# Kernel tuning notes

Measured on AMD Instinct MI355X. Metric: run time of the kernel, lower is better.

The kernel has to match this reference:

```python
import jax, jax.numpy as jnp
import numpy as np

D_MODEL, N_HEADS, D_HEAD = 768, 12, 64
BATCH, SEQ = 4, 2048
INIT_STD = 0.02


def setup_inputs() -> dict:
    key = jax.random.key(0)
    ks = jax.random.split(key, 5)
    x = jax.random.normal(ks[0], (BATCH, SEQ, D_MODEL), dtype=jnp.float32)
    W_Q = INIT_STD * jax.random.normal(ks[1], (N_HEADS, D_MODEL, D_HEAD), dtype=jnp.float32)
    W_K = INIT_STD * jax.random.normal(ks[2], (N_HEADS, D_MODEL, D_HEAD), dtype=jnp.float32)
    W_V = INIT_STD * jax.random.normal(ks[3], (N_HEADS, D_MODEL, D_HEAD), dtype=jnp.float32)
    W_O = INIT_STD * jax.random.normal(ks[4], (N_HEADS, D_HEAD, D_MODEL), dtype=jnp.float32)
    b_Q = jnp.zeros((N_HEADS, D_HEAD), dtype=jnp.float32)
    b_K = jnp.zeros((N_HEADS, D_HEAD), dtype=jnp.float32)
    b_V = jnp.zeros((N_HEADS, D_HEAD), dtype=jnp.float32)
    b_O = jnp.zeros((D_MODEL,), dtype=jnp.float32)
    return {"x": x, "W_Q": W_Q, "W_K": W_K, "W_V": W_V, "W_O": W_O,
            "b_Q": b_Q, "b_K": b_K, "b_V": b_V, "b_O": b_O}


def reference(x, W_Q, W_K, W_V, W_O, b_Q, b_K, b_V, b_O):
    # projections: [b,s,e] x [n,e,h] -> [b,s,n,h]
    q = jnp.einsum('bse,neh->bsnh', x, W_Q) + b_Q
    k = jnp.einsum('bse,neh->bsnh', x, W_K) + b_K
    v = jnp.einsum('bse,neh->bsnh', x, W_V) + b_V
    scores = jnp.einsum('bqnh,bknh->bnqk', q, k) / np.float32(np.sqrt(D_HEAD))
    S = x.shape[1]
    causal = jnp.tril(jnp.ones((S, S), dtype=bool))  # True where allowed
    scores = jnp.where(causal, scores, -jnp.inf)
    pattern = jax.nn.softmax(scores, axis=-1)
    z = jnp.einsum('bnqk,bknh->bqnh', pattern, v)
    # combine heads: sum over n of z @ W_O
    attn_out = jnp.einsum('bqnh,nhe->bqe', z, W_O) + b_O
    return attn_out
```

## Files before the change

kernel.cpp:

```cpp
#include <hip/hip_runtime.h>
#include <hip/hip_bf16.h>

typedef short s16x8 __attribute__((ext_vector_type(8)));
typedef short s16x4 __attribute__((ext_vector_type(4)));
typedef float f32x4 __attribute__((ext_vector_type(4)));
typedef __hip_bfloat16 bf16;

#define MFMA16(a, b, c) __builtin_amdgcn_mfma_f32_16x16x32_bf16((a), (b), (c), 0, 0, 0)

#define BATCH 4
#define SEQ 2048
#define NH 12
#define DH 64
#define DM 768
#define ROWS (BATCH * SEQ)
#define QKVC (3 * DM)
#define LOG2E 1.4426950408889634f

static __device__ inline float fast_exp2(float x) {
  float r;
  asm("v_exp_f32 %0, %1" : "=v"(r) : "v"(x));
  return r;
}
static __device__ inline unsigned pkbf16(float a, float b) {
  bf16 ha = __float2bfloat16(a), hb = __float2bfloat16(b);
  unsigned short ua, ub;
  __builtin_memcpy(&ua, &ha, 2);
  __builtin_memcpy(&ub, &hb, 2);
  return (unsigned)ua | ((unsigned)ub << 16);
}

typedef __attribute__((address_space(3))) unsigned int lds_u32;
typedef __attribute__((address_space(1))) const unsigned int glb_u32;
static __device__ inline void gl2lds16(const void* g, void* l) {
  __builtin_amdgcn_global_load_lds((glb_u32*)g, (lds_u32*)l, 16, 0, 0);
}

#define NWC (QKVC * DM)
#define NWO (DM * DM)
#define NXC (ROWS * DM / 8)
__global__ __launch_bounds__(256) void prep_all(
    const float* __restrict__ wq, const float* __restrict__ wk,
    const float* __restrict__ wv, const float* __restrict__ wo,
    const float* __restrict__ x, bf16* __restrict__ WcT,
    bf16* __restrict__ WoT, bf16* __restrict__ xb) {
  int i = blockIdx.x * 256 + threadIdx.x;
  if (i < NWC) {
    int c = i / DM, e = i % DM;
    int mat = c / DM;
    int r = c % DM;
    int n = r >> 6, h = r & 63;
    const float* W = (mat == 0) ? wq : ((mat == 1) ? wk : wv);
    WcT[i] = __float2bfloat16(W[n * (DM * DH) + e * DH + h]);
  } else if (i < NWC + NWO) {
    int j = i - NWC;
    int e = j / DM, r = j % DM;
    WoT[j] = __float2bfloat16(wo[r * DM + e]);
  } else {
    int j = i - NWC - NWO;
    const float* src = x + (size_t)j * 8;
    float4 f0 = *(const float4*)src;
    float4 f1 = *(const float4*)(src + 4);
    bf16 tmp[8];
    tmp[0] = __float2bfloat16(f0.x); tmp[1] = __float2bfloat16(f0.y);
    tmp[2] = __float2bfloat16(f0.z); tmp[3] = __float2bfloat16(f0.w);
    tmp[4] = __float2bfloat16(f1.x); tmp[5] = __float2bfloat16(f1.y);
    tmp[6] = __float2bfloat16(f1.z); tmp[7] = __float2bfloat16(f1.w);
    *(s16x8*)(xb + (size_t)j * 8) = *(const s16x8*)tmp;
  }
}

__global__ __launch_bounds__(256) void qkv_gemm(
    const bf16* __restrict__ xb, const bf16* __restrict__ WcT,
    const float* __restrict__ bQ, const float* __restrict__ bK,
    const float* __restrict__ bV, bf16* __restrict__ Qb,
    bf16* __restrict__ Kb, bf16* __restrict__ Vt) {
  __shared__ bf16 As[128 * 32];
  __shared__ bf16 Bs[128 * 32];
  const int m0 = blockIdx.x * 128;
  const int n0 = blockIdx.y * 128;
  const int tid = threadIdx.x;
  const int wave = tid >> 6, lane = tid & 63;
  const int quad = lane >> 4, l15 = lane & 15;
  const int wm = (wave & 1) * 64, wn = (wave >> 1) * 64;

  f32x4 acc[4][4] = {};

  for (int k0 = 0; k0 < DM; k0 += 32) {
    {
      int c = tid, row = c >> 2, sg = (c & 3) << 3;
      gl2lds16(xb + (size_t)(m0 + row) * DM + k0 + sg, &As[c * 8]);
      gl2lds16(WcT + (size_t)(n0 + row) * DM + k0 + sg, &Bs[c * 8]);
      c = tid + 256; row = c >> 2; sg = (c & 3) << 3;
      gl2lds16(xb + (size_t)(m0 + row) * DM + k0 + sg, &As[c * 8]);
      gl2lds16(WcT + (size_t)(n0 + row) * DM + k0 + sg, &Bs[c * 8]);
    }
    __syncthreads();
    s16x8 af[4], bfr[4];
    for (int i = 0; i < 4; i++)
      af[i] = *(const s16x8*)&As[(wm + i * 16 + l15) * 32 + quad * 8];
    for (int j = 0; j < 4; j++)
      bfr[j] = *(const s16x8*)&Bs[(wn + j * 16 + l15) * 32 + quad * 8];
    for (int i = 0; i < 4; i++)
      for (int j = 0; j < 4; j++)
        acc[i][j] = MFMA16(af[i], bfr[j], acc[i][j]);
    __syncthreads();
  }

  const int mat = n0 / DM;
  for (int j = 0; j < 4; j++) {
    int col = n0 + wn + j * 16 + l15;
    int cc = col - mat * DM;
    int head = cc >> 6, h = cc & 63;
    float bsv = ((mat == 0) ? bQ : (mat == 1) ? bK : bV)[cc];
    for (int i = 0; i < 4; i++) {
      int row0 = m0 + wm + i * 16 + quad * 4;
      int b = row0 >> 11;
      int s = row0 & 2047;
      int bh = b * NH + head;
      if (mat == 2) {
        s16x4 pv;
        for (int r = 0; r < 4; r++) {
          bf16 hv = __float2bfloat16(acc[i][j][r] + bsv);
          short sv; __builtin_memcpy(&sv, &hv, 2);
          pv[r] = sv;
        }
        *(s16x4*)(Vt + ((size_t)bh * DH + h) * SEQ + s) = pv;
      } else {
        const float scale = (mat == 0) ? (0.125f * LOG2E) : 1.0f;
        bf16* dst = ((mat == 0) ? Qb : Kb) + ((size_t)bh * SEQ + s) * DH + h;
        for (int r = 0; r < 4; r++)
          dst[(size_t)r * DH] = __float2bfloat16((acc[i][j][r] + bsv) * scale);
      }
    }
  }
}

__global__ __launch_bounds__(256) void flash_kernel(
    const bf16* __restrict__ Qb, const bf16* __restrict__ Kb,
    const bf16* __restrict__ Vt, bf16* __restrict__ Z) {
  __shared__ bf16 Ks[64 * 72];
  __shared__ bf16 VsT[64 * 72];
  __shared__ bf16 Ps[4][16 * 72];

  const int bh = blockIdx.x >> 4;
  const int p = blockIdx.x & 15;
  const int qtA = 31 - p, qtB = p;
  const int b = bh / NH, head = bh % NH;
  const int tid = threadIdx.x;
  const int wave = tid >> 6, lane = tid & 63;
  const int quad = lane >> 4, l15 = lane & 15;
  const int qwA = qtA * 64 + wave * 16;
  const int qwB = qtB * 64 + wave * 16;

  const bf16* Kbase = Kb + (size_t)bh * SEQ * DH;
  const bf16* Vbase = Vt + (size_t)bh * DH * SEQ;

  s16x8 bqA[2], bqB[2];
  for (int ks = 0; ks < 2; ks++) {
    bqA[ks] = *(const s16x8*)(Qb +
        ((size_t)bh * SEQ + qwA + l15) * DH + ks * 32 + quad * 8);
    bqB[ks] = *(const s16x8*)(Qb +
        ((size_t)bh * SEQ + qwB + l15) * DH + ks * 32 + quad * 8);
  }

  f32x4 oA[4] = {}, oB[4] = {};
  float lA = 0.f, lB = 0.f;

  s16x8 kr[2], vr[2];
  auto load_tile = [&](int kt) {
    const int kbase = kt * 64;
    for (int u = 0; u < 2; u++) {
      int c = tid + u * 256;
      int row = c >> 3, seg = (c & 7) << 3;
      kr[u] = *(const s16x8*)(Kbase + (size_t)(kbase + row) * DH + seg);
      vr[u] = *(const s16x8*)(Vbase + (size_t)row * SEQ + kbase + seg);
    }
  };
  auto store_tile = [&]() {
    for (int u = 0; u < 2; u++) {
      int c = tid + u * 256;
      int row = c >> 3, seg = (c & 7) << 3;
      *(s16x8*)&Ks[row * 72 + seg] = kr[u];
      *(s16x8*)&VsT[row * 72 + seg] = vr[u];
    }
  };

  auto compute = [&](int kt, const s16x8 bq[2], f32x4 o[4], float& l_i,
                     int qw, bool diag) {
    const int kbase = kt * 64;
    f32x4 s[4] = {};
    for (int ks = 0; ks < 2; ks++) {
      s16x8 ak[4];
      for (int ktf = 0; ktf < 4; ktf++)
        ak[ktf] = *(const s16x8*)&Ks[(ktf * 16 + l15) * 72 + ks * 32 + quad * 8];
      for (int ktf = 0; ktf < 4; ktf++)
        s[ktf] = MFMA16(ak[ktf], bq[ks], s[ktf]);
    }

    if (diag) {
      int qg = qw + l15;
      for (int ktf = 0; ktf < 4; ktf++)
        for (int r = 0; r < 4; r++) {
          int kg = kbase + ktf * 16 + quad * 4 + r;
          if (kg > qg) s[ktf][r] = -1e30f;
        }
    }

    float rs = 0.f;
    for (int ktf = 0; ktf < 4; ktf++)
      for (int r = 0; r < 4; r++) {
        float pv = fast_exp2(s[ktf][r]);
        s[ktf][r] = pv;
        rs += pv;
      }
    l_i += rs;

    bf16* Pw = Ps[wave];
    for (int ktf = 0; ktf < 4; ktf++) {
      uint2 w;
      w.x = pkbf16(s[ktf][0], s[ktf][1]);
      w.y = pkbf16(s[ktf][2], s[ktf][3]);
      *(uint2*)&Pw[l15 * 72 + ktf * 16 + quad * 4] = w;
    }
    asm volatile("s_waitcnt lgkmcnt(0)" ::: "memory");

    for (int ks2 = 0; ks2 < 2; ks2++) {
      s16x8 ap = *(const s16x8*)&Pw[l15 * 72 + ks2 * 32 + quad * 8];
      for (int hf = 0; hf < 4; hf++) {
        s16x8 bv =
            *(const s16x8*)&VsT[(hf * 16 + l15) * 72 + ks2 * 32 + quad * 8];
        o[hf] = MFMA16(ap, bv, o[hf]);
      }
    }
  };

  load_tile(0);
  for (int kt = 0; kt <= qtA; kt++) {
    __syncthreads();
    store_tile();
    __syncthreads();
    if (kt < qtA) load_tile(kt + 1);
    compute(kt, bqA, oA, lA, qwA, kt == qtA);
    if (kt <= qtB) compute(kt, bqB, oB, lB, qwB, kt == qtB);
  }

  auto epilogue = [&](f32x4 o[4], float l_i, int qw) {
    float lv = l_i;
    lv += __shfl_xor(lv, 16, 64);
    lv += __shfl_xor(lv, 32, 64);
    float linv = 1.f / lv;
    for (int r = 0; r < 4; r++) {
      float li = __shfl(linv, (lane & 48) | (quad * 4 + r), 64);
      int q = qw + quad * 4 + r;
      for (int hf = 0; hf < 4; hf++) {
        Z[((size_t)b * SEQ + q) * DM + head * DH + hf * 16 + l15] =
            __float2bfloat16(o[hf][r] * li);
      }
    }
  };
  epilogue(oA, lA, qwA);
  epilogue(oB, lB, qwB);
}

__global__ __launch_bounds__(256) void out_gemm(
    const bf16* __restrict__ Z, const bf16* __restrict__ WoT,
    const float* __restrict__ bO, float* __restrict__ out) {
  __shared__ bf16 As[128 * 32];
  __shared__ bf16 Bs[128 * 32];
  const int m0 = blockIdx.x * 128;
  const int n0 = blockIdx.y * 128;
  const int tid = threadIdx.x;
  const int wave = tid >> 6, lane = tid & 63;
  const int quad = lane >> 4, l15 = lane & 15;
  const int wm = (wave & 1) * 64, wn = (wave >> 1) * 64;

  f32x4 acc[4][4] = {};

  for (int k0 = 0; k0 < DM; k0 += 32) {
    {
      int c = tid, row = c >> 2, sg = (c & 3) << 3;
      gl2lds16(Z + (size_t)(m0 + row) * DM + k0 + sg, &As[c * 8]);
      gl2lds16(WoT + (size_t)(n0 + row) * DM + k0 + sg, &Bs[c * 8]);
      c = tid + 256; row = c >> 2; sg = (c & 3) << 3;
      gl2lds16(Z + (size_t)(m0 + row) * DM + k0 + sg, &As[c * 8]);
      gl2lds16(WoT + (size_t)(n0 + row) * DM + k0 + sg, &Bs[c * 8]);
    }
    __syncthreads();
    s16x8 af[4], bfr[4];
    for (int i = 0; i < 4; i++)
      af[i] = *(const s16x8*)&As[(wm + i * 16 + l15) * 32 + quad * 8];
    for (int j = 0; j < 4; j++)
      bfr[j] = *(const s16x8*)&Bs[(wn + j * 16 + l15) * 32 + quad * 8];
    for (int i = 0; i < 4; i++)
      for (int j = 0; j < 4; j++)
        acc[i][j] = MFMA16(af[i], bfr[j], acc[i][j]);
    __syncthreads();
  }

  for (int j = 0; j < 4; j++) {
    int col = n0 + wn + j * 16 + l15;
    float bv = bO[col];
    for (int i = 0; i < 4; i++)
      for (int r = 0; r < 4; r++) {
        int row = m0 + wm + i * 16 + quad * 4 + r;
        out[(size_t)row * DM + col] = acc[i][j][r] + bv;
      }
  }
}

extern "C" void kernel_launch(void* const* d_in, const int* in_sizes, int n_in,
                              void* d_out, int out_size, void* d_ws,
                              size_t ws_size, hipStream_t stream) {
  const float* x  = (const float*)d_in[0];
  const float* wq = (const float*)d_in[1];
  const float* wk = (const float*)d_in[2];
  const float* wv = (const float*)d_in[3];
  const float* wo = (const float*)d_in[4];
  const float* bq = (const float*)d_in[5];
  const float* bk = (const float*)d_in[6];
  const float* bv = (const float*)d_in[7];
  const float* bo = (const float*)d_in[8];
  float* out = (float*)d_out;

  bf16* WcT = (bf16*)d_ws;
  bf16* WoT = WcT + (size_t)QKVC * DM;
  bf16* Qb  = WoT + (size_t)DM * DM;
  bf16* Kb  = Qb + (size_t)ROWS * DM;
  bf16* Vt  = Kb + (size_t)ROWS * DM;
  bf16* xbZ = Vt + (size_t)ROWS * DM;

  prep_all<<<(NWC + NWO + NXC) / 256, 256, 0, stream>>>(
      wq, wk, wv, wo, x, WcT, WoT, xbZ);
  qkv_gemm<<<dim3(ROWS / 128, QKVC / 128), 256, 0, stream>>>(
      xbZ, WcT, bq, bk, bv, Qb, Kb, Vt);
  flash_kernel<<<48 * 16, 256, 0, stream>>>(Qb, Kb, Vt, xbZ);
  out_gemm<<<dim3(ROWS / 128, DM / 128), 256, 0, stream>>>(xbZ, WoT, bo, out);
}
```

Measured before the change: 220.0 us.

## Transpose P via permlane swaps instead of LDS and remap blocks per XCD

The softmax probabilities are packed to bf16 and rearranged into the MFMA A-operand layout with permlane32/permlane16 swap instructions, replacing the per-wave LDS staging buffer, its write/read, and the lgkmcnt wait. Block indices are also remapped so that the blocks working on the same batch-head land on the same XCD, which aims to improve L2 reuse of K/V. This removes LDS traffic and a sync point from the inner loop. It relies on the permlane swap lane mapping exactly matching the previous LDS layout.

```diff
diff --git a/kernel.cpp b/kernel.cpp
--- a/kernel.cpp
+++ b/kernel.cpp
@@ -141,10 +141,11 @@
     const bf16* __restrict__ Vt, bf16* __restrict__ Z) {
   __shared__ bf16 Ks[64 * 72];
   __shared__ bf16 VsT[64 * 72];
-  __shared__ bf16 Ps[4][16 * 72];
-
-  const int bh = blockIdx.x >> 4;
-  const int p = blockIdx.x & 15;
+
+  const int xcd = blockIdx.x & 7;
+  const int slot = blockIdx.x >> 3;
+  const int bh = xcd * 6 + (slot >> 4);
+  const int p = slot & 15;
   const int qtA = 31 - p, qtB = p;
   const int b = bh / NH, head = bh % NH;
   const int tid = threadIdx.x;
@@ -208,29 +209,36 @@
     }
 
     float rs = 0.f;
-    for (int ktf = 0; ktf < 4; ktf++)
-      for (int r = 0; r < 4; r++) {
-        float pv = fast_exp2(s[ktf][r]);
-        s[ktf][r] = pv;
-        rs += pv;
-      }
+    unsigned w[4][2];
+    for (int ktf = 0; ktf < 4; ktf++) {
+      float p0 = fast_exp2(s[ktf][0]);
+      float p1 = fast_exp2(s[ktf][1]);
+      float p2 = fast_exp2(s[ktf][2]);
+      float p3 = fast_exp2(s[ktf][3]);
+      rs += (p0 + p1) + (p2 + p3);
+      w[ktf][0] = pkbf16(p0, p1);
+      w[ktf][1] = pkbf16(p2, p3);
+    }
     l_i += rs;
 
-    bf16* Pw = Ps[wave];
-    for (int ktf = 0; ktf < 4; ktf++) {
-      uint2 w;
-      w.x = pkbf16(s[ktf][0], s[ktf][1]);
-      w.y = pkbf16(s[ktf][2], s[ktf][3]);
-      *(uint2*)&Pw[l15 * 72 + ktf * 16 + quad * 4] = w;
-    }
-    asm volatile("s_waitcnt lgkmcnt(0)" ::: "memory");
-
+    s16x8 ap[2];
     for (int ks2 = 0; ks2 < 2; ks2++) {
-      s16x8 ap = *(const s16x8*)&Pw[l15 * 72 + ks2 * 32 + quad * 8];
+      int dw[4];
+      for (int j = 0; j < 2; j++) {
+        auto t = __builtin_amdgcn_permlane32_swap(
+            (int)w[2 * ks2][j], (int)w[2 * ks2 + 1][j], false, false);
+        auto pq = __builtin_amdgcn_permlane16_swap(t[0], t[1], false, false);
+        dw[j] = pq[0];
+        dw[2 + j] = pq[1];
+      }
+      __builtin_memcpy(&ap[ks2], dw, 16);
+    }
+
+    for (int ks2 = 0; ks2 < 2; ks2++) {
       for (int hf = 0; hf < 4; hf++) {
         s16x8 bv =
             *(const s16x8*)&VsT[(hf * 16 + l15) * 72 + ks2 * 32 + quad * 8];
-        o[hf] = MFMA16(ap, bv, o[hf]);
+        o[hf] = MFMA16(ap[ks2], bv, o[hf]);
       }
     }
   };
```

Result: slower. 230.6 us (+4.8%).
